# Performance work log

Measured on AMD Instinct MI355X. Metric: run time of the kernel, lower is better.

The kernel has to match this reference:

```python
import jax, jax.numpy as jnp
import numpy as np

# ---- grid / frustum config (from default grid_config & data_config) ----
DB = (1.0, 60.0, 1.0)                 # dbound
OGH, OGW, DS = 256, 704, 16           # input size, downsample
FH, FW = OGH // DS, OGW // DS         # 16, 44
DEPTH = int(round((DB[1] - DB[0]) / DB[2]))  # 59 depth bins
NX0, NX1, NZ = 128, 128, 1            # BEV grid
DX = np.array([0.8, 0.8, 20.0], np.float32)
BX = np.array([-51.2 + 0.4, -51.2 + 0.4, 0.0], np.float32)  # row0 + dx/2


def _frustum():
    # (D, FH, FW, 3): pixel (u, v, depth)
    ds = jnp.broadcast_to(jnp.arange(DB[0], DB[1], DB[2], dtype=jnp.float32).reshape(-1, 1, 1), (DEPTH, FH, FW))
    xs = jnp.broadcast_to(jnp.linspace(0.0, OGW - 1.0, FW, dtype=jnp.float32).reshape(1, 1, FW), (DEPTH, FH, FW))
    ys = jnp.broadcast_to(jnp.linspace(0.0, OGH - 1.0, FH, dtype=jnp.float32).reshape(1, FH, 1), (DEPTH, FH, FW))
    return jnp.stack([xs, ys, ds], axis=-1)


def _geometry(rots, trans, intrins, post_rots, post_trans, bda):
    # pixel frustum -> ego-frame 3D points; (B, N, D, FH, FW, 3)
    pts = _frustum() - post_trans[:, :, None, None, None, :]
    pts = jnp.einsum('bnij,bndhwj->bndhwi', jnp.linalg.inv(post_rots), pts)
    pts = jnp.concatenate([pts[..., :2] * pts[..., 2:3], pts[..., 2:3]], axis=-1)
    comb = jnp.einsum('bnij,bnjk->bnik', rots, jnp.linalg.inv(intrins))
    pts = jnp.einsum('bnij,bndhwj->bndhwi', comb, pts) + trans[:, :, None, None, None, :]
    pts = jnp.einsum('bij,bndhwj->bndhwi', bda, pts)
    return pts


def _voxel_pool(geom, vol):
    # geom: (B,N,D,FH,FW,3), vol: (B,N,D,FH,FW,C) -> BEV (B, C*NZ, NX0, NX1)
    B, C = vol.shape[0], vol.shape[-1]
    gidx = jnp.floor((geom - (BX - DX / 2.0)) / DX).astype(jnp.int32)
    kept = ((gidx[..., 0] >= 0) & (gidx[..., 0] < NX0)
            & (gidx[..., 1] >= 0) & (gidx[..., 1] < NX1)
            & (gidx[..., 2] >= 0) & (gidx[..., 2] < NZ))
    bidx = jnp.broadcast_to(jnp.arange(B, dtype=jnp.int32).reshape(B, 1, 1, 1, 1), gidx.shape[:-1])
    flat = ((bidx * NZ + gidx[..., 2]) * NX0 + gidx[..., 0]) * NX1 + gidx[..., 1]
    nvox = B * NZ * NX0 * NX1
    flat = jnp.where(kept, flat, nvox).reshape(-1)      # dump bucket for culled pts
    feats = vol.reshape(-1, C)
    bev = jax.ops.segment_sum(feats, flat, num_segments=nvox + 1)[:nvox]
    bev = bev.reshape(B, NZ, NX0, NX1, C)
    bev = jnp.moveaxis(bev, -1, 2).reshape(B, NZ * C, NX0, NX1)  # z-major channel cat
    return bev


def setup_inputs() -> dict:
    key = jax.random.key(0)
    B, N, CIN, CT = 4, 6, 512, 64
    k1, k2 = jax.random.split(key, 2)
    x = jax.random.normal(k1, (B, N, CIN, FH, FW), dtype=jnp.float32)
    weight = jax.random.normal(k2, (DEPTH + CT, CIN), dtype=jnp.float32) * 0.02
    bias = jnp.zeros((DEPTH + CT,), dtype=jnp.float32)
    # cam->ego rotation (cam z forward -> ego x, cam x right -> ego -y, cam y down -> ego -z)
    Rcam = jnp.asarray(np.array([[0., 0., 1.], [-1., 0., 0.], [0., -1., 0.]], np.float32))
    rots = jnp.tile(Rcam, (B, N, 1, 1))
    trans = jnp.zeros((B, N, 3), dtype=jnp.float32)
    K = jnp.asarray(np.array([[600., 0., 352.], [0., 600., 128.], [0., 0., 1.]], np.float32))
    intrins = jnp.tile(K, (B, N, 1, 1))
    post_rots = jnp.tile(jnp.eye(3, dtype=jnp.float32), (B, N, 1, 1))
    post_trans = jnp.zeros((B, N, 3), dtype=jnp.float32)
    bda = jnp.tile(jnp.eye(3, dtype=jnp.float32), (B, 1, 1))
    return dict(x=x, rots=rots, trans=trans, intrins=intrins, post_rots=post_rots,
                post_trans=post_trans, bda=bda, weight=weight, bias=bias)


def reference(x, rots, trans, intrins, post_rots, post_trans, bda, weight, bias):
    # 1x1 depth/context head (eval mode): (B,N,Cin,H,W) -> (B,N,D+C,H,W)
    out = jnp.einsum('bnchw,oc->bnohw', x, weight) + bias[None, None, :, None, None]
    depth = jax.nn.softmax(out[:, :, :DEPTH], axis=2)      # (B,N,D,H,W)
    feat = out[:, :, DEPTH:]                               # (B,N,C,H,W)
    # depth-context outer product -> frustum volume (B,N,D,H,W,C)
    vol = jnp.einsum('bndhw,bnchw->bndhwc', depth, feat)
    geom = _geometry(rots, trans, intrins, post_rots, post_trans, bda)
    bev = _voxel_pool(geom, vol)                           # (B, C*NZ, 128, 128)
    return bev, depth
```

## Files before the change

kernel.cpp:

```cpp
#include <hip/hip_runtime.h>
#include <math.h>

#define CIN   512
#define NOUT  123
#define DEPN  59
#define CT    64
#define B_    4
#define N_    6
#define FH    16
#define FW    44
#define HW    704
#define NPIX  (B_*N_*HW)
#define NX    128
#define BEV_ELEMS (B_*CT*NX*NX)
#define DEPTH_OFF BEV_ELEMS

#define TDREC   40
#define WS_WB   1920
#define WS_PS   (WS_WB + 32768)
#define WS_FS   (WS_PS + NPIX*64)

typedef short bf16x8 __attribute__((ext_vector_type(8)));
typedef float f32x4  __attribute__((ext_vector_type(4)));

__device__ inline unsigned short f2bf(float f) {
    unsigned u = __float_as_uint(f);
    return (unsigned short)((u + 0x7fffu + ((u >> 16) & 1u)) >> 16);
}

__device__ inline void inv3d(const double* m, double* o) {
    #pragma clang fp contract(off)
    double c00 = m[4]*m[8] - m[5]*m[7];
    double c01 = m[5]*m[6] - m[3]*m[8];
    double c02 = m[3]*m[7] - m[4]*m[6];
    double det = m[0]*c00 + m[1]*c01 + m[2]*c02;
    o[0] = c00/det; o[1] = (m[2]*m[7]-m[1]*m[8])/det; o[2] = (m[1]*m[5]-m[2]*m[4])/det;
    o[3] = c01/det; o[4] = (m[0]*m[8]-m[2]*m[6])/det; o[5] = (m[2]*m[3]-m[0]*m[5])/det;
    o[6] = c02/det; o[7] = (m[1]*m[6]-m[0]*m[7])/det; o[8] = (m[0]*m[4]-m[1]*m[3])/det;
}
__device__ inline void mm3d(const double* a, const double* b, double* o) {
    #pragma clang fp contract(off)
    for (int i = 0; i < 3; ++i)
        for (int k = 0; k < 3; ++k)
            o[i*3+k] = (a[i*3+0]*b[0*3+k] + a[i*3+1]*b[1*3+k]) + a[i*3+2]*b[2*3+k];
}

__global__ void k0_prep(const float* __restrict__ rots, const float* __restrict__ trans,
                        const float* __restrict__ intr, const float* __restrict__ prots,
                        const float* __restrict__ ptrans, const float* __restrict__ bda,
                        const float* __restrict__ W, float* __restrict__ ws,
                        float* __restrict__ dout) {
    int tid = blockIdx.x * 256 + threadIdx.x;
    int stride = gridDim.x * 256;
    float4 z = {0.f, 0.f, 0.f, 0.f};
    for (int i = tid; i < BEV_ELEMS / 4; i += stride)
        *(float4*)(dout + 4 * (size_t)i) = z;
    unsigned short* wb = (unsigned short*)(ws + WS_WB);
    for (int i = tid; i < 128 * CIN; i += stride) {
        int o = i >> 9, c = i & 511;
        wb[i] = (o < NOUT) ? f2bf(W[o * CIN + c]) : (unsigned short)0;
    }
    if (blockIdx.x == 0 && threadIdx.x < B_ * N_) {
        #pragma clang fp contract(off)
        int t = threadIdx.x;
        int b = t / N_;
        double* X = (double*)(ws) + t * TDREC;
        double PR[9], Kd[9], Rd[9], Bd[9];
        for (int i = 0; i < 9; ++i) PR[i] = (double)prots[t * 9 + i];
        for (int i = 0; i < 9; ++i) Kd[i] = (double)intr[t * 9 + i];
        for (int i = 0; i < 9; ++i) Rd[i] = (double)rots[t * 9 + i];
        for (int i = 0; i < 9; ++i) Bd[i] = (double)bda[b * 9 + i];
        double iPR[9]; inv3d(PR, iPR);
        for (int i = 0; i < 9; ++i) X[i] = iPR[i];
        for (int i = 0; i < 3; ++i) X[9 + i] = (double)ptrans[t * 3 + i];
        double iK[9];  inv3d(Kd, iK);
        double comb[9]; mm3d(Rd, iK, comb);
        for (int i = 0; i < 9; ++i) X[12 + i] = comb[i];
        for (int i = 0; i < 3; ++i) X[21 + i] = (double)trans[t * 3 + i];
        for (int i = 0; i < 9; ++i) X[24 + i] = Bd[i];
    }
}

#define K1A   (64 * 72)
#define K1T   (K1A + 128 * 72)
__global__ __launch_bounds__(512) void k1_gemm(const float* __restrict__ x,
                                               const float* __restrict__ bias,
                                               float* __restrict__ ws,
                                               float* __restrict__ dout) {
    __shared__ __align__(16) unsigned short smem[2][2][K1T];
    const int tid = threadIdx.x;
    const int grp = tid >> 8;
    const int gtid = tid & 255;
    const int wave = gtid >> 6;
    const int lane = tid & 63;
    const int l15 = lane & 15, quad = lane >> 4;
    const int bn = blockIdx.y;
    const int pixbase = blockIdx.x * 64;
    const float* xg = x + (size_t)bn * CIN * HW + pixbase;
    const unsigned short* wbg = (const unsigned short*)(ws + WS_WB);
    const int cpack = gtid >> 4;
    const int pix4 = (gtid & 15) * 4;
    const int wo  = gtid >> 3;
    const int wsub = gtid & 7;
    const int ck0 = grp * 256;

    f32x4 acc[8] = {};
    float4 r0, r1, r2, r3;
    uint4  w4[4];

    {
        const float* src = xg + (size_t)(ck0 + 4 * cpack) * HW + pix4;
        r0 = *(const float4*)(src);
        r1 = *(const float4*)(src + HW);
        r2 = *(const float4*)(src + 2 * HW);
        r3 = *(const float4*)(src + 3 * HW);
        #pragma unroll
        for (int i = 0; i < 4; ++i)
            w4[i] = *(const uint4*)(wbg + (size_t)(wo + 32 * i) * CIN + ck0 + wsub * 8);
    }

    #pragma unroll
    for (int it = 0; it < 4; ++it) {
        const int buf = it & 1;
        unsigned short* sa = smem[grp][buf];
        unsigned short* sb = smem[grp][buf] + K1A;
        {
            const float* f0 = (const float*)&r0; const float* f1 = (const float*)&r1;
            const float* f2 = (const float*)&r2; const float* f3 = (const float*)&r3;
            #pragma unroll
            for (int i = 0; i < 4; ++i) {
                uint2 pk;
                pk.x = (unsigned)f2bf(f0[i]) | ((unsigned)f2bf(f1[i]) << 16);
                pk.y = (unsigned)f2bf(f2[i]) | ((unsigned)f2bf(f3[i]) << 16);
                *(uint2*)&sa[(pix4 + i) * 72 + 4 * cpack] = pk;
            }
            #pragma unroll
            for (int i = 0; i < 4; ++i)
                *(uint4*)&sb[(wo + 32 * i) * 72 + wsub * 8] = w4[i];
        }
        if (it < 3) {
            const int ck = ck0 + (it + 1) * 64;
            const float* src = xg + (size_t)(ck + 4 * cpack) * HW + pix4;
            r0 = *(const float4*)(src);
            r1 = *(const float4*)(src + HW);
            r2 = *(const float4*)(src + 2 * HW);
            r3 = *(const float4*)(src + 3 * HW);
            #pragma unroll
            for (int i = 0; i < 4; ++i)
                w4[i] = *(const uint4*)(wbg + (size_t)(wo + 32 * i) * CIN + ck + wsub * 8);
        }
        __syncthreads();
        #pragma unroll
        for (int ks = 0; ks < 64; ks += 32) {
            const bf16x8 a = *(const bf16x8*)&sa[(wave * 16 + l15) * 72 + ks + quad * 8];
            #pragma unroll
            for (int nt = 0; nt < 8; ++nt) {
                const bf16x8 b = *(const bf16x8*)&sb[(nt * 16 + l15) * 72 + ks + quad * 8];
                acc[nt] = __builtin_amdgcn_mfma_f32_16x16x32_bf16(a, b, acc[nt], 0, 0, 0);
            }
        }
    }

    __syncthreads();
    float* red = (float*)&smem[0][0][0];
    if (grp == 1) {
        #pragma unroll
        for (int nt = 0; nt < 8; ++nt)
            #pragma unroll
            for (int reg = 0; reg < 4; ++reg)
                red[(wave * 16 + quad * 4 + reg) * 132 + nt * 16 + l15] = acc[nt][reg];
    }
    __syncthreads();
    if (grp == 0) {
        #pragma unroll
        for (int nt = 0; nt < 8; ++nt)
            #pragma unroll
            for (int reg = 0; reg < 4; ++reg)
                acc[nt][reg] += red[(wave * 16 + quad * 4 + reg) * 132 + nt * 16 + l15];
    }
    __syncthreads();

    float* sred = (float*)&smem[0][0][0];
    const int b = bn / N_, n = bn - b * N_;
    if (grp == 0) {
        float bb[8];
        #pragma unroll
        for (int nt = 0; nt < 8; ++nt) {
            int o = nt * 16 + l15;
            bb[nt] = (o < NOUT) ? bias[o] : 0.0f;
        }
        float* ps = ws + WS_PS;
        float* fs = ws + WS_FS;
        #pragma unroll
        for (int reg = 0; reg < 4; ++reg) {
            int pixl = wave * 16 + quad * 4 + reg;
            int pix = pixbase + pixl;
            int h = pix / FW, w = pix - h * FW;
            size_t row = (size_t)(b * FW + w) * 96 + n * FH + h;
            float v[4]; float m = -INFINITY;
            #pragma unroll
            for (int nt = 0; nt < 4; ++nt) {
                v[nt] = acc[nt][reg] + bb[nt];
                if (nt * 16 + l15 < DEPN) m = fmaxf(m, v[nt]);
            }
            #pragma unroll
            for (int msk = 8; msk >= 1; msk >>= 1) m = fmaxf(m, __shfl_xor(m, msk, 64));
            float e[4], s = 0.0f;
            #pragma unroll
            for (int nt = 0; nt < 4; ++nt) {
                e[nt] = (nt * 16 + l15 < DEPN) ? expf(v[nt] - m) : 0.0f;
                s += e[nt];
            }
            #pragma unroll
            for (int msk = 8; msk >= 1; msk >>= 1) s += __shfl_xor(s, msk, 64);
            const float inv = 1.0f / s;
            #pragma unroll
            for (int nt = 0; nt < 4; ++nt) {
                int o = nt * 16 + l15;
                if (o < DEPN) {
                    float p = e[nt] * inv;
                    ps[row * 64 + o] = p;
                    sred[pixl * 65 + o] = p;
                } else fs[row * 64 + (o - DEPN)] = v[nt];
            }
            #pragma unroll
            for (int nt = 4; nt < 8; ++nt) {
                int o = nt * 16 + l15;
                if (o < NOUT) fs[row * 64 + (o - DEPN)] = acc[nt][reg] + bb[nt];
            }
        }
    }
    __syncthreads();
    const int wv8 = tid >> 6;
    for (int o = wv8; o < DEPN; o += 8)
        dout[DEPTH_OFF + ((size_t)bn * DEPN + o) * HW + pixbase + lane] = sred[lane * 65 + o];
}

#define DQ2 16
__global__ __launch_bounds__(256) void k2b_geom(float* __restrict__ ws,
                                                float* __restrict__ dout) {
    __shared__ float sF[96][64];
    __shared__ float sP[DQ2][97];
    __shared__ unsigned short sv16[DQ2 * 96];
    __shared__ double sT[N_ * TDREC];
    __shared__ int sflag[DQ2];
    const int tid = threadIdx.x;
    const int bw = blockIdx.x;
    const int b = bw / FW, w = bw - b * FW;
    const int dbase = blockIdx.y * DQ2;
    const int nd = min(DQ2, DEPN - dbase);

    {
        const float* fsrc = ws + WS_FS + (size_t)bw * (96 * 64);
        const float* psrc = ws + WS_PS + (size_t)bw * (96 * 64);
        for (int i = tid; i < 96 * 16; i += 256) {
            int j = i >> 4, c4 = (i & 15) * 4;
            *(float4*)&sF[j][c4] = *(const float4*)(fsrc + j * 64 + c4);
        }
        for (int i = tid; i < 96 * 4; i += 256) {
            int j = i >> 2, q = i & 3;
            const float4 p4 = *(const float4*)(psrc + j * 64 + dbase + 4 * q);
            sP[4 * q + 0][j] = p4.x; sP[4 * q + 1][j] = p4.y;
            sP[4 * q + 2][j] = p4.z; sP[4 * q + 3][j] = p4.w;
        }
        if (tid < N_ * TDREC) sT[tid] = ((const double*)ws)[b * (N_ * TDREC) + tid];
    }
    __syncthreads();

    {
        #pragma clang fp contract(off)
        const double xs = (w == 43) ? 703.0 : (double)w * (703.0 / 43.0);
        const double BXY = (double)(-51.2000007629394531f);
        for (int idx = tid; idx < nd * 96; idx += 256) {
            int dl = idx / 96, j = idx - dl * 96;
            int n = j >> 4, h = j & 15;
            const double* T = &sT[n * TDREC];
            const double ys = (double)(h * 17);
            const double u0 = xs - T[9];
            const double u1 = ys - T[10];
            const double u2 = (double)(dbase + dl + 1) - T[11];
            const double p0 = (T[0]*u0 + T[1]*u1) + T[2]*u2;
            const double p1 = (T[3]*u0 + T[4]*u1) + T[5]*u2;
            const double p2 = (T[6]*u0 + T[7]*u1) + T[8]*u2;
            const double q0 = p0 * p2, q1 = p1 * p2, q2 = p2;
            const double r0 = ((T[12]*q0 + T[13]*q1) + T[14]*q2) + T[21];
            const double r1 = ((T[15]*q0 + T[16]*q1) + T[17]*q2) + T[22];
            const double r2 = ((T[18]*q0 + T[19]*q1) + T[20]*q2) + T[23];
            const double g0 = (T[24]*r0 + T[25]*r1) + T[26]*r2;
            const double g1 = (T[27]*r0 + T[28]*r1) + T[29]*r2;
            const double g2 = (T[30]*r0 + T[31]*r1) + T[32]*r2;
            const double fx = floor((g0 - BXY) / 0.8);
            const double fy = floor((g1 - BXY) / 0.8);
            const bool keep = (fx >= 0.0) & (fx < 128.0) & (fy >= 0.0) & (fy < 128.0) &
                              (g2 >= -10.0) & (g2 < 10.0);
            sv16[idx] = keep ? (unsigned short)((int)fx * NX + (int)fy) : (unsigned short)0xFFFF;
        }
    }
    __syncthreads();

    if (tid < nd) {
        int u = -1; bool mix = false;
        for (int j = 0; j < 96; ++j) {
            int v = sv16[tid * 96 + j];
            if (v != 0xFFFF) { if (u < 0) u = v; else if (v != u) mix = true; }
        }
        sflag[tid] = mix ? -2 : u;
    }
    for (int idx = tid; idx < nd * 96; idx += 256) {
        if (sv16[idx] == 0xFFFF) {
            int dl = idx / 96, j = idx - dl * 96;
            sP[dl][j] = 0.0f;
        }
    }
    __syncthreads();

    const int dl = tid >> 4, ci = tid & 15;
    if (dl < nd && sflag[dl] >= 0) {
        float a0 = 0.f, a1 = 0.f, a2 = 0.f, a3 = 0.f;
        for (int j = 0; j < 96; ++j) {
            const float p = sP[dl][j];
            const float4 f4 = *(const float4*)&sF[j][4 * ci];
            a0 = fmaf(p, f4.x, a0); a1 = fmaf(p, f4.y, a1);
            a2 = fmaf(p, f4.z, a2); a3 = fmaf(p, f4.w, a3);
        }
        float* dst = dout + (((size_t)(b * CT + 4 * ci)) << 14) + sflag[dl];
        atomicAdd(dst,                 a0);
        atomicAdd(dst + (1 << 14),     a1);
        atomicAdd(dst + (2 << 14),     a2);
        atomicAdd(dst + (3 << 14),     a3);
    }
    for (int d2 = 0; d2 < nd; ++d2) {
        if (sflag[d2] == -2) {
            int c = tid & 63, g = tid >> 6;
            for (int jj = 0; jj < 24; ++jj) {
                int j = g * 24 + jj;
                int v = sv16[d2 * 96 + j];
                if (v != 0xFFFF)
                    atomicAdd(dout + (((size_t)(b * CT + c)) << 14) + v,
                              sP[d2][j] * sF[j][c]);
            }
        }
    }
}

extern "C" void kernel_launch(void* const* d_in, const int* in_sizes, int n_in,
                              void* d_out, int out_size, void* d_ws, size_t ws_size,
                              hipStream_t stream) {
    const float* x      = (const float*)d_in[0];
    const float* rots   = (const float*)d_in[1];
    const float* trans  = (const float*)d_in[2];
    const float* intr   = (const float*)d_in[3];
    const float* prots  = (const float*)d_in[4];
    const float* ptrans = (const float*)d_in[5];
    const float* bda    = (const float*)d_in[6];
    const float* W      = (const float*)d_in[7];
    const float* bias   = (const float*)d_in[8];
    float* out = (float*)d_out;
    float* ws  = (float*)d_ws;

    k0_prep<<<512, 256, 0, stream>>>(rots, trans, intr, prots, ptrans, bda, W, ws, out);
    k1_gemm<<<dim3(HW / 64, B_ * N_), 512, 0, stream>>>(x, bias, ws, out);
    k2b_geom<<<dim3(B_ * FW, 4), 256, 0, stream>>>(ws, out);
}
```

Before: 168.4 us.

## Precompute per-ray depth-polynomial geometry coefficients and streamline geom pooling kernel

Adds a small kernel that, for each (batch, width, camera, height) ray, folds the full frustum-to-ego transform into quadratic-in-depth coefficients. The pooling kernel then evaluates a quadratic per depth bin instead of the full chain of double-precision matrix products. The per-depth uniform-voxel check becomes a parallel shuffle reduction, and the weighted reduction loop is vectorised over four pixels at a time. The change adds an extra kernel launch and extra workspace traffic. Reassociating the double-precision math and replacing the division by 0.8 with a multiply by 1.25 can shift floor boundaries for points right at voxel edges.

```diff
diff --git a/kernel.cpp b/kernel.cpp
--- a/kernel.cpp
+++ b/kernel.cpp
@@ -19,6 +19,7 @@
 #define WS_WB   1920
 #define WS_PS   (WS_WB + 32768)
 #define WS_FS   (WS_PS + NPIX*64)
+#define WS_GC   (WS_FS + NPIX*64)
 
 typedef short bf16x8 __attribute__((ext_vector_type(8)));
 typedef float f32x4  __attribute__((ext_vector_type(4)));
@@ -79,6 +80,45 @@
         for (int i = 0; i < 3; ++i) X[21 + i] = (double)trans[t * 3 + i];
         for (int i = 0; i < 9; ++i) X[24 + i] = Bd[i];
     }
+}
+
+__global__ __launch_bounds__(256) void k0b_coef(float* __restrict__ ws) {
+    #pragma clang fp contract(off)
+    int i = blockIdx.x * 256 + threadIdx.x;
+    int b = i / (FW * 96);
+    int rem = i - b * (FW * 96);
+    int w = rem / 96;
+    int j = rem - w * 96;
+    int n = j >> 4, h = j & 15;
+    const double* T = (const double*)(ws) + (b * N_ + n) * TDREC;
+    const double xs = (w == 43) ? 703.0 : (double)w * (703.0 / 43.0);
+    const double ys = (double)(h * 17);
+    const double u0 = xs - T[9];
+    const double u1 = ys - T[10];
+    double pA[3], pB[3];
+    #pragma unroll
+    for (int k = 0; k < 3; ++k) {
+        pA[k] = (T[3*k]*u0 + T[3*k+1]*u1) - T[3*k+2]*T[11];
+        pB[k] = T[3*k+2];
+    }
+    double q0c[3] = { pA[0]*pA[2], pA[0]*pB[2] + pB[0]*pA[2], pB[0]*pB[2] };
+    double q1c[3] = { pA[1]*pA[2], pA[1]*pB[2] + pB[1]*pA[2], pB[1]*pB[2] };
+    double q2c[3] = { pA[2], pB[2], 0.0 };
+    double rc[3][3], gc[3][3];
+    #pragma unroll
+    for (int r = 0; r < 3; ++r)
+        #pragma unroll
+        for (int k = 0; k < 3; ++k)
+            rc[r][k] = ((T[12+3*r]*q0c[k] + T[13+3*r]*q1c[k]) + T[14+3*r]*q2c[k])
+                       + ((k == 0) ? T[21+r] : 0.0);
+    #pragma unroll
+    for (int g = 0; g < 3; ++g)
+        #pragma unroll
+        for (int k = 0; k < 3; ++k)
+            gc[g][k] = (T[24+3*g]*rc[0][k] + T[25+3*g]*rc[1][k]) + T[26+3*g]*rc[2][k];
+    double* dst = (double*)(ws) + WS_GC / 2 + (size_t)i * 9;
+    #pragma unroll
+    for (int t = 0; t < 9; ++t) dst[t] = gc[t / 3][t % 3];
 }
 
 #define K1A   (64 * 72)
@@ -240,13 +280,13 @@
 __global__ __launch_bounds__(256) void k2b_geom(float* __restrict__ ws,
                                                 float* __restrict__ dout) {
     __shared__ float sF[96][64];
-    __shared__ float sP[DQ2][97];
+    __shared__ float sP[DQ2][100];
     __shared__ unsigned short sv16[DQ2 * 96];
-    __shared__ double sT[N_ * TDREC];
+    __shared__ __align__(16) double sG[96 * 9];
     __shared__ int sflag[DQ2];
     const int tid = threadIdx.x;
     const int bw = blockIdx.x;
-    const int b = bw / FW, w = bw - b * FW;
+    const int b = bw / FW;
     const int dbase = blockIdx.y * DQ2;
     const int nd = min(DQ2, DEPN - dbase);
 
@@ -263,34 +303,24 @@
             sP[4 * q + 0][j] = p4.x; sP[4 * q + 1][j] = p4.y;
             sP[4 * q + 2][j] = p4.z; sP[4 * q + 3][j] = p4.w;
         }
-        if (tid < N_ * TDREC) sT[tid] = ((const double*)ws)[b * (N_ * TDREC) + tid];
+        const double2* gsrc = (const double2*)((const double*)(ws) + WS_GC / 2
+                                               + (size_t)bw * (96 * 9));
+        for (int i = tid; i < 432; i += 256)
+            ((double2*)sG)[i] = gsrc[i];
     }
     __syncthreads();
 
     {
-        #pragma clang fp contract(off)
-        const double xs = (w == 43) ? 703.0 : (double)w * (703.0 / 43.0);
         const double BXY = (double)(-51.2000007629394531f);
         for (int idx = tid; idx < nd * 96; idx += 256) {
             int dl = idx / 96, j = idx - dl * 96;
-            int n = j >> 4, h = j & 15;
-            const double* T = &sT[n * TDREC];
-            const double ys = (double)(h * 17);
-            const double u0 = xs - T[9];
-            const double u1 = ys - T[10];
-            const double u2 = (double)(dbase + dl + 1) - T[11];
-            const double p0 = (T[0]*u0 + T[1]*u1) + T[2]*u2;
-            const double p1 = (T[3]*u0 + T[4]*u1) + T[5]*u2;
-            const double p2 = (T[6]*u0 + T[7]*u1) + T[8]*u2;
-            const double q0 = p0 * p2, q1 = p1 * p2, q2 = p2;
-            const double r0 = ((T[12]*q0 + T[13]*q1) + T[14]*q2) + T[21];
-            const double r1 = ((T[15]*q0 + T[16]*q1) + T[17]*q2) + T[22];
-            const double r2 = ((T[18]*q0 + T[19]*q1) + T[20]*q2) + T[23];
-            const double g0 = (T[24]*r0 + T[25]*r1) + T[26]*r2;
-            const double g1 = (T[27]*r0 + T[28]*r1) + T[29]*r2;
-            const double g2 = (T[30]*r0 + T[31]*r1) + T[32]*r2;
-            const double fx = floor((g0 - BXY) / 0.8);
-            const double fy = floor((g1 - BXY) / 0.8);
+            const double* G = &sG[j * 9];
+            const double dsv = (double)(dbase + dl + 1);
+            const double g0 = (G[2] * dsv + G[1]) * dsv + G[0];
+            const double g1 = (G[5] * dsv + G[4]) * dsv + G[3];
+            const double g2 = (G[8] * dsv + G[7]) * dsv + G[6];
+            const double fx = floor((g0 - BXY) * 1.25);
+            const double fy = floor((g1 - BXY) * 1.25);
             const bool keep = (fx >= 0.0) & (fx < 128.0) & (fy >= 0.0) & (fy < 128.0) &
                               (g2 >= -10.0) & (g2 < 10.0);
             sv16[idx] = keep ? (unsigned short)((int)fx * NX + (int)fy) : (unsigned short)0xFFFF;
@@ -298,13 +328,23 @@
     }
     __syncthreads();
 
-    if (tid < nd) {
-        int u = -1; bool mix = false;
-        for (int j = 0; j < 96; ++j) {
-            int v = sv16[tid * 96 + j];
-            if (v != 0xFFFF) { if (u < 0) u = v; else if (v != u) mix = true; }
-        }
-        sflag[tid] = mix ? -2 : u;
+    {
+        const int dl = tid >> 4, s = tid & 15;
+        int u = -1, mix = 0;
+        const int base = dl * 96 + s * 6;
+        #pragma unroll
+        for (int t = 0; t < 6; ++t) {
+            int v = sv16[base + t];
+            if (v != 0xFFFF) { if (u < 0) u = v; else if (v != u) mix = 1; }
+        }
+        #pragma unroll
+        for (int msk = 1; msk < 16; msk <<= 1) {
+            int uo = __shfl_xor(u, msk, 64);
+            int mo = __shfl_xor(mix, msk, 64);
+            mix = mix | mo | ((u >= 0 && uo >= 0 && uo != u) ? 1 : 0);
+            u = (u < 0) ? uo : u;
+        }
+        if (s == 0 && dl < nd) sflag[dl] = mix ? -2 : u;
     }
     for (int idx = tid; idx < nd * 96; idx += 256) {
         if (sv16[idx] == 0xFFFF) {
@@ -316,18 +356,27 @@
 
     const int dl = tid >> 4, ci = tid & 15;
     if (dl < nd && sflag[dl] >= 0) {
-        float a0 = 0.f, a1 = 0.f, a2 = 0.f, a3 = 0.f;
-        for (int j = 0; j < 96; ++j) {
-            const float p = sP[dl][j];
-            const float4 f4 = *(const float4*)&sF[j][4 * ci];
-            a0 = fmaf(p, f4.x, a0); a1 = fmaf(p, f4.y, a1);
-            a2 = fmaf(p, f4.z, a2); a3 = fmaf(p, f4.w, a3);
+        float ax = 0.f, ay = 0.f, az = 0.f, aw = 0.f;
+        for (int jj = 0; jj < 96; jj += 4) {
+            const float4 pv = *(const float4*)&sP[dl][jj];
+            const float4 f0 = *(const float4*)&sF[jj + 0][4 * ci];
+            const float4 f1 = *(const float4*)&sF[jj + 1][4 * ci];
+            const float4 f2 = *(const float4*)&sF[jj + 2][4 * ci];
+            const float4 f3 = *(const float4*)&sF[jj + 3][4 * ci];
+            ax = fmaf(pv.x, f0.x, ax); ay = fmaf(pv.x, f0.y, ay);
+            az = fmaf(pv.x, f0.z, az); aw = fmaf(pv.x, f0.w, aw);
+            ax = fmaf(pv.y, f1.x, ax); ay = fmaf(pv.y, f1.y, ay);
+            az = fmaf(pv.y, f1.z, az); aw = fmaf(pv.y, f1.w, aw);
+            ax = fmaf(pv.z, f2.x, ax); ay = fmaf(pv.z, f2.y, ay);
+            az = fmaf(pv.z, f2.z, az); aw = fmaf(pv.z, f2.w, aw);
+            ax = fmaf(pv.w, f3.x, ax); ay = fmaf(pv.w, f3.y, ay);
+            az = fmaf(pv.w, f3.z, az); aw = fmaf(pv.w, f3.w, aw);
         }
         float* dst = dout + (((size_t)(b * CT + 4 * ci)) << 14) + sflag[dl];
-        atomicAdd(dst,                 a0);
-        atomicAdd(dst + (1 << 14),     a1);
-        atomicAdd(dst + (2 << 14),     a2);
-        atomicAdd(dst + (3 << 14),     a3);
+        atomicAdd(dst,             ax);
+        atomicAdd(dst + (1 << 14), ay);
+        atomicAdd(dst + (2 << 14), az);
+        atomicAdd(dst + (3 << 14), aw);
     }
     for (int d2 = 0; d2 < nd; ++d2) {
         if (sflag[d2] == -2) {
@@ -359,6 +408,7 @@
     float* ws  = (float*)d_ws;
 
     k0_prep<<<512, 256, 0, stream>>>(rots, trans, intr, prots, ptrans, bda, W, ws, out);
+    k0b_coef<<<66, 256, 0, stream>>>(ws);
     k1_gemm<<<dim3(HW / 64, B_ * N_), 512, 0, stream>>>(x, bias, ws, out);
     k2b_geom<<<dim3(B_ * FW, 4), 256, 0, stream>>>(ws, out);
 }
```

Result: faster. 161.1 us (-4.4%).
